# Optimization experiments

Measured on AMD Instinct MI355X. Metric: run time of the kernel, lower is better.

Reference implementation:

```python
import jax, jax.numpy as jnp
import numpy as np

N = 100000   # nodes
E = 600000   # edges per edge set
D = 128      # d_graph_layer (= num_features)
ED = 3       # edge_dim
DF = 512     # d_FC_layer
B = 64       # graphs in batch
C = 2        # num_classes
NL = 3       # n_graph_layer (stacked convs)


def _lin_params(key, out_d, in_d, bias=True, scale=0.05):
    kw, kb = jax.random.split(key)
    w = jax.random.normal(kw, (out_d, in_d), dtype=jnp.float32) * scale
    b = jax.random.normal(kb, (out_d,), dtype=jnp.float32) * scale if bias else None
    return w, b


def setup_inputs() -> dict:
    key = jax.random.key(0)
    ks = jax.random.split(key, 32)
    inp = {}
    inp["x"] = jax.random.normal(ks[0], (N, D), dtype=jnp.float32)
    inp["edge_index1"] = jax.random.randint(ks[1], (2, E), 0, N, dtype=jnp.int64) if jax.config.jax_enable_x64 else jax.random.randint(ks[1], (2, E), 0, N).astype(jnp.int32)
    inp["edge_index2"] = jax.random.randint(ks[2], (2, E), 0, N).astype(inp["edge_index1"].dtype)
    inp["edge_attr1"] = jax.random.normal(ks[3], (E, ED), dtype=jnp.float32)
    inp["edge_attr2"] = jax.random.normal(ks[4], (E, ED), dtype=jnp.float32)
    inp["flexible_idx"] = jnp.ones((N,), dtype=bool)
    inp["batchs"] = jnp.sort(jax.random.randint(ks[5], (N,), 0, B)).astype(inp["edge_index1"].dtype)

    # conv1 params: lin_query, lin_key, lin_value (with bias), lin_edge (no bias), lin_skip (bias)
    inp["c1_wq"], inp["c1_bq"] = _lin_params(ks[6], D, D)
    inp["c1_wk"], inp["c1_bk"] = _lin_params(ks[7], D, D)
    inp["c1_wv"], inp["c1_bv"] = _lin_params(ks[8], D, D)
    inp["c1_we"], _ = _lin_params(ks[9], D, ED, bias=False)
    inp["c1_ws"], inp["c1_bs"] = _lin_params(ks[10], D, D)

    # stacked convs: [NL, ...]
    def stack(kbase, out_d, in_d, bias=True):
        ws, bs = [], []
        for i in range(NL):
            w, b = _lin_params(jax.random.fold_in(kbase, i), out_d, in_d, bias)
            ws.append(w)
            bs.append(b)
        return jnp.stack(ws), (jnp.stack(bs) if bias else None)
    inp["cs_wq"], inp["cs_bq"] = stack(ks[11], D, D)
    inp["cs_wk"], inp["cs_bk"] = stack(ks[12], D, D)
    inp["cs_wv"], inp["cs_bv"] = stack(ks[13], D, D)
    inp["cs_we"], _ = stack(ks[14], D, ED, bias=False)
    inp["cs_ws"], inp["cs_bs"] = stack(ks[15], D, D)

    inp["lin0_w"], inp["lin0_b"] = _lin_params(ks[16], DF, D)
    inp["lin1_w"], inp["lin1_b"] = _lin_params(ks[17], DF, DF)
    inp["lin3_w"], inp["lin3_b"] = _lin_params(ks[18], C, DF)
    return inp


def _tconv(x, edge_index, edge_attr, wq, bq, wk, bk, wv, bv, we, ws, bs):
    """PyG TransformerConv, heads=1, concat=True, root_weight=True, edge_dim=3."""
    n = x.shape[0]
    src, dst = edge_index[0], edge_index[1]
    q = x @ wq.T + bq                     # [N, D]
    k = x @ wk.T + bk                     # [N, D]
    v = x @ wv.T + bv                     # [N, D]
    e = edge_attr @ we.T                  # [E, D]
    k_e = k[src] + e                      # [E, D]
    v_e = v[src] + e                      # [E, D]
    scale = 1.0 / jnp.sqrt(jnp.asarray(x.shape[-1], x.dtype))
    logits = jnp.sum(q[dst] * k_e, axis=-1) * scale   # [E]
    m = jax.ops.segment_max(logits, dst, num_segments=n)
    w = jnp.exp(logits - m[dst])
    den = jax.ops.segment_sum(w, dst, num_segments=n)
    alpha = w / (den[dst] + 1e-16)        # softmax over incoming edges
    out = jax.ops.segment_sum(alpha[:, None] * v_e, dst, num_segments=n)
    return out + x @ ws.T + bs            # root / skip connection


def reference(x, edge_index1, edge_index2, edge_attr1, edge_attr2, flexible_idx, batchs,
              c1_wq, c1_bq, c1_wk, c1_bk, c1_wv, c1_bv, c1_we, c1_ws, c1_bs,
              cs_wq, cs_bq, cs_wk, cs_bk, cs_wv, cs_bv, cs_we, cs_ws, cs_bs,
              lin0_w, lin0_b, lin1_w, lin1_b, lin3_w, lin3_b):
    # conv1 applied to both edge structures; x = relu(conv(g2)) - relu(conv(g1))
    x1 = jax.nn.relu(_tconv(x, edge_index1, edge_attr1, c1_wq, c1_bq, c1_wk, c1_bk, c1_wv, c1_bv, c1_we, c1_ws, c1_bs))
    x2 = jax.nn.relu(_tconv(x, edge_index2, edge_attr2, c1_wq, c1_bq, c1_wk, c1_bk, c1_wv, c1_bv, c1_we, c1_ws, c1_bs))
    h = x2 - x1                           # dropout_rate=0 -> identity
    for i in range(NL):
        x1 = jax.nn.relu(_tconv(h, edge_index1, edge_attr1, cs_wq[i], cs_bq[i], cs_wk[i], cs_bk[i], cs_wv[i], cs_bv[i], cs_we[i], cs_ws[i], cs_bs[i]))
        x2 = jax.nn.relu(_tconv(h, edge_index2, edge_attr2, cs_wq[i], cs_bq[i], cs_wk[i], cs_bk[i], cs_wv[i], cs_bv[i], cs_we[i], cs_ws[i], cs_bs[i]))
        h = x2 - x1
    # global_mean_pool (flexible=False)
    sums = jax.ops.segment_sum(h, batchs, num_segments=B)               # [B, D]
    cnt = jax.ops.segment_sum(jnp.ones((h.shape[0],), h.dtype), batchs, num_segments=B)
    g = sums / jnp.maximum(cnt, 1.0)[:, None]
    g = jax.nn.relu(g @ lin0_w.T + lin0_b)
    g = jax.nn.relu(g @ lin1_w.T + lin1_b)
    logits = g @ lin3_w.T + lin3_b
    return jax.nn.log_softmax(logits, axis=1)   # last == 'log'
```

## Files before the change

### kernel.cpp

```cpp
#include <hip/hip_runtime.h>

#define NNODES 100000
#define NEDGES 600000
#define DIM    128
#define NB     64
#define DFC    512
#define NB1    391

typedef __attribute__((ext_vector_type(8))) short short8v;
typedef __attribute__((ext_vector_type(4))) float float4v;

__device__ __forceinline__ float bf2f(unsigned short u) {
    return __uint_as_float((unsigned)u << 16);
}
__device__ __forceinline__ unsigned short f2bf(float f) {
    unsigned u = __float_as_uint(f);
    return (unsigned short)((u + 0x7FFF + ((u >> 16) & 1)) >> 16);
}

__global__ __launch_bounds__(256) void wsplit_kernel(
    const float* __restrict__ c1q, const float* __restrict__ c1k,
    const float* __restrict__ c1v, const float* __restrict__ c1s,
    const float* __restrict__ csq, const float* __restrict__ csk,
    const float* __restrict__ csv, const float* __restrict__ css,
    short* __restrict__ whi, short* __restrict__ wlo)
{
    int t = blockIdx.x * 256 + threadIdx.x;
    int mat = t >> 11;
    int tt = t & 2047;
    int lane = tt & 63, nt = (tt >> 6) & 7, ks = tt >> 9;
    int li = mat >> 2, mm = mat & 3;
    const float* W;
    if (li == 0) W = (mm == 0) ? c1q : (mm == 1) ? c1k : (mm == 2) ? c1v : c1s;
    else {
        const float* base = (mm == 0) ? csq : (mm == 1) ? csk : (mm == 2) ? csv : css;
        W = base + (size_t)(li - 1) * 16384;
    }
    int n = nt * 16 + (lane & 15);
    int k0 = ks * 32 + (lane >> 4) * 8;
    size_t ob = (size_t)mat * 16384 + (size_t)((ks * 8 + nt) * 64 + lane) * 8;
#pragma unroll
    for (int j = 0; j < 8; ++j) {
        float w = W[n * 128 + k0 + j];
        unsigned ub = __float_as_uint(w);
        float lo = w - __uint_as_float(ub & 0xFFFF0000u);
        whi[ob + j] = (short)(ub >> 16);
        wlo[ob + j] = (short)(__float_as_uint(lo) >> 16);
    }
}

__global__ __launch_bounds__(256) void qkvs_mfma_kernel(
    const float* __restrict__ x,
    const short* __restrict__ whi, const short* __restrict__ wlo,
    const float* __restrict__ bq, const float* __restrict__ bk,
    const float* __restrict__ bv, const float* __restrict__ bs,
    float* __restrict__ q, unsigned short* __restrict__ k16,
    unsigned short* __restrict__ v16,
    float* __restrict__ o1, float* __restrict__ h2)
{
    const int lane = threadIdx.x & 63;
    const int m = threadIdx.x >> 6;
    const int r0 = blockIdx.x * 32;
    const int lrow = lane & 15;
    const int lgrp = lane >> 4;

    float4v acc[2][8] = {};
    const short* Whi = whi + (size_t)m * 16384;
    const short* Wlo = wlo + (size_t)m * 16384;

    for (int ks = 0; ks < 4; ++ks) {
        short8v ahi[2], alo[2];
#pragma unroll
        for (int mt = 0; mt < 2; ++mt) {
            const float* xp = x + (size_t)(r0 + mt * 16 + lrow) * DIM + ks * 32 + lgrp * 8;
            float4 xa = *(const float4*)xp;
            float4 xb = *(const float4*)(xp + 4);
            float xs[8] = {xa.x, xa.y, xa.z, xa.w, xb.x, xb.y, xb.z, xb.w};
#pragma unroll
            for (int j = 0; j < 8; ++j) {
                unsigned ub = __float_as_uint(xs[j]);
                float lo = xs[j] - __uint_as_float(ub & 0xFFFF0000u);
                ahi[mt][j] = (short)(ub >> 16);
                alo[mt][j] = (short)(__float_as_uint(lo) >> 16);
            }
        }
        const short* bh = Whi + (size_t)((ks * 8) * 64 + lane) * 8;
        const short* bl = Wlo + (size_t)((ks * 8) * 64 + lane) * 8;
#pragma unroll
        for (int nt = 0; nt < 8; ++nt) {
            short8v bhi = *(const short8v*)(bh + (size_t)nt * 512);
            short8v blo = *(const short8v*)(bl + (size_t)nt * 512);
#pragma unroll
            for (int mt = 0; mt < 2; ++mt) {
                acc[mt][nt] = __builtin_amdgcn_mfma_f32_16x16x32_bf16(ahi[mt], bhi, acc[mt][nt], 0, 0, 0);
                acc[mt][nt] = __builtin_amdgcn_mfma_f32_16x16x32_bf16(ahi[mt], blo, acc[mt][nt], 0, 0, 0);
                acc[mt][nt] = __builtin_amdgcn_mfma_f32_16x16x32_bf16(alo[mt], bhi, acc[mt][nt], 0, 0, 0);
            }
        }
    }

    __syncthreads();

    const float* bias = (m == 0) ? bq : (m == 1) ? bk : (m == 2) ? bv : bs;
#pragma unroll
    for (int nt = 0; nt < 8; ++nt) {
        float bvv = bias[nt * 16 + lrow];
#pragma unroll
        for (int mt = 0; mt < 2; ++mt) {
#pragma unroll
            for (int i = 0; i < 4; ++i) {
                int row = r0 + mt * 16 + lgrp * 4 + i;
                float val = acc[mt][nt][i] + bvv;
                size_t off = (size_t)row * DIM + nt * 16 + lrow;
                if (m == 0) q[off] = val;
                else if (m == 1) k16[off] = f2bf(val);
                else if (m == 2) v16[off] = f2bf(val);
                else { o1[off] = val; h2[off] = val; }
            }
        }
    }
}

__global__ __launch_bounds__(256) void hist_kernel(const int* __restrict__ ei,
                                                   int* __restrict__ deg) {
    int e = blockIdx.x * 256 + threadIdx.x;
    if (e < NEDGES) atomicAdd(&deg[ei[NEDGES + e]], 1);
}

__global__ __launch_bounds__(256) void scan1_kernel(const int* __restrict__ deg,
                                                    int* __restrict__ excl,
                                                    int* __restrict__ bsum) {
    __shared__ int s[256];
    const int tid = threadIdx.x;
    const int i = blockIdx.x * 256 + tid;
    const int v = (i < NNODES) ? deg[i] : 0;
    s[tid] = v;
    __syncthreads();
    for (int off = 1; off < 256; off <<= 1) {
        int t = (tid >= off) ? s[tid - off] : 0;
        __syncthreads();
        s[tid] += t;
        __syncthreads();
    }
    if (i < NNODES) excl[i] = s[tid] - v;
    if (tid == 255) bsum[blockIdx.x] = s[255];
}

__global__ __launch_bounds__(512) void scan2_kernel(int* __restrict__ bsum) {
    __shared__ int s[512];
    const int tid = threadIdx.x;
    const int v = (tid < NB1) ? bsum[tid] : 0;
    s[tid] = v;
    __syncthreads();
    for (int off = 1; off < 512; off <<= 1) {
        int t = (tid >= off) ? s[tid - off] : 0;
        __syncthreads();
        s[tid] += t;
        __syncthreads();
    }
    if (tid < NB1) bsum[tid] = s[tid] - v;
}

__global__ __launch_bounds__(256) void scan3_kernel(const int* __restrict__ excl,
                                                    const int* __restrict__ bsum,
                                                    int* __restrict__ rowptr) {
    const int i = blockIdx.x * 256 + threadIdx.x;
    if (i < NNODES) rowptr[i] = excl[i] + bsum[blockIdx.x];
    if (i == 0) rowptr[NNODES] = NEDGES;
}

__global__ __launch_bounds__(256) void scatter_edges_kernel(
    const int* __restrict__ ei, const int* __restrict__ rowptr,
    int* __restrict__ fill, int2* __restrict__ sse) {
    int e = blockIdx.x * 256 + threadIdx.x;
    if (e >= NEDGES) return;
    int dst = ei[NEDGES + e];
    int pos = rowptr[dst] + atomicAdd(&fill[dst], 1);
    sse[pos] = make_int2(ei[e], e);
}

__global__ __launch_bounds__(256) void attn_aggregate_kernel(
    const int* __restrict__ rowptr1, const int2* __restrict__ sse1,
    const float* __restrict__ ea1,
    const int* __restrict__ rowptr2, const int2* __restrict__ sse2,
    const float* __restrict__ ea2,
    const float* __restrict__ we,
    const float* __restrict__ q, const unsigned short* __restrict__ k16,
    const unsigned short* __restrict__ v16,
    float* __restrict__ o1, float* __restrict__ o2)
{
    const int wave = threadIdx.x >> 6;
    const int lane = threadIdx.x & 63;
    const int idx = blockIdx.x * 4 + wave;
    if (idx >= 2 * NNODES) return;
    const int g = (idx >= NNODES) ? 1 : 0;
    const int d = idx - (g ? NNODES : 0);

    const int*   rowptr = g ? rowptr2 : rowptr1;
    const int2*  sse    = g ? sse2 : sse1;
    const float* ea     = g ? ea2 : ea1;
    float*       out    = g ? o2 : o1;

    const int p0 = rowptr[d], p1 = rowptr[d + 1];
    if (p0 == p1) return;

    const int c0 = lane, c1 = lane + 64;
    const float w00 = we[c0 * 3 + 0], w01 = we[c0 * 3 + 1], w02 = we[c0 * 3 + 2];
    const float w10 = we[c1 * 3 + 0], w11 = we[c1 * 3 + 1], w12 = we[c1 * 3 + 2];
    const float scale = 0.08838834764831845f;
    const float q0 = q[(size_t)d * DIM + c0] * scale;
    const float q1 = q[(size_t)d * DIM + c1] * scale;

    float m = -INFINITY, den = 0.f, a0 = 0.f, a1 = 0.f;

    for (int p = p0; p < p1; p += 4) {
        const int nn = p1 - p;
        float l[4], vv0[4], vv1[4];
#pragma unroll
        for (int j = 0; j < 4; ++j) {
            if (j < nn) {
                const int2 sv = sse[p + j];
                const int src = sv.x;
                const float ea0 = ea[sv.y * 3 + 0];
                const float ea1v = ea[sv.y * 3 + 1];
                const float ea2v = ea[sv.y * 3 + 2];
                const float ep0 = fmaf(ea0, w00, fmaf(ea1v, w01, ea2v * w02));
                const float ep1 = fmaf(ea0, w10, fmaf(ea1v, w11, ea2v * w12));
                const unsigned short* kp = k16 + (size_t)src * DIM;
                const unsigned short* vp = v16 + (size_t)src * DIM;
                const float k0 = bf2f(kp[c0]) + ep0;
                const float k1 = bf2f(kp[c1]) + ep1;
                vv0[j] = bf2f(vp[c0]) + ep0;
                vv1[j] = bf2f(vp[c1]) + ep1;
                l[j] = fmaf(q0, k0, q1 * k1);
            } else {
                l[j] = -INFINITY;
                vv0[j] = 0.f;
                vv1[j] = 0.f;
            }
        }
#pragma unroll
        for (int off = 32; off > 0; off >>= 1) {
#pragma unroll
            for (int j = 0; j < 4; ++j) l[j] += __shfl_xor(l[j], off, 64);
        }
        const float cm = fmaxf(fmaxf(l[0], l[1]), fmaxf(l[2], l[3]));
        const float mn = fmaxf(m, cm);
        const float sc = __expf(m - mn);
        const float e0 = __expf(l[0] - mn), e1 = __expf(l[1] - mn);
        const float e2 = __expf(l[2] - mn), e3 = __expf(l[3] - mn);
        den = den * sc + ((e0 + e1) + (e2 + e3));
        a0 = a0 * sc + ((e0 * vv0[0] + e1 * vv0[1]) + (e2 * vv0[2] + e3 * vv0[3]));
        a1 = a1 * sc + ((e0 * vv1[0] + e1 * vv1[1]) + (e2 * vv1[2] + e3 * vv1[3]));
        m = mn;
    }
    const float inv = 1.f / (den + 1e-16f);
    out[(size_t)d * DIM + c0] += a0 * inv;
    out[(size_t)d * DIM + c1] += a1 * inv;
}

__global__ __launch_bounds__(256) void combine_kernel(
    const float4* __restrict__ o1, float4* __restrict__ h)
{
    const int i = blockIdx.x * 256 + threadIdx.x;
    float4 a = o1[i];
    float4 b = h[i];
    float4 r;
    r.x = fmaxf(b.x, 0.f) - fmaxf(a.x, 0.f);
    r.y = fmaxf(b.y, 0.f) - fmaxf(a.y, 0.f);
    r.z = fmaxf(b.z, 0.f) - fmaxf(a.z, 0.f);
    r.w = fmaxf(b.w, 0.f) - fmaxf(a.w, 0.f);
    h[i] = r;
}

__global__ __launch_bounds__(256) void pool_kernel(
    const float* __restrict__ h, const int* __restrict__ batchs,
    float* __restrict__ sums, float* __restrict__ cnt)
{
    const int sub = threadIdx.x >> 7;
    const int c = threadIdx.x & 127;
    int n0 = blockIdx.x * 32 + sub * 16;
    int nend = n0 + 16;
    if (nend > NNODES) nend = NNODES;
    float acc = 0.f, ccnt = 0.f;
    int curb = -1;
    for (int nd = n0; nd < nend; ++nd) {
        int b = batchs[nd];
        if (b != curb) {
            if (curb >= 0) {
                atomicAdd(&sums[curb * DIM + c], acc);
                if (c == 0) atomicAdd(&cnt[curb], ccnt);
            }
            acc = 0.f; ccnt = 0.f; curb = b;
        }
        acc += h[(size_t)nd * DIM + c];
        ccnt += 1.f;
    }
    if (curb >= 0) {
        atomicAdd(&sums[curb * DIM + c], acc);
        if (c == 0) atomicAdd(&cnt[curb], ccnt);
    }
}

__global__ __launch_bounds__(256) void head_kernel(
    const float* __restrict__ sums, const float* __restrict__ cnt,
    const float* __restrict__ l0w, const float* __restrict__ l0b,
    const float* __restrict__ l1w, const float* __restrict__ l1b,
    const float* __restrict__ l3w, const float* __restrict__ l3b,
    float* __restrict__ out)
{
    __shared__ float g[DIM];
    __shared__ float h0[DFC];
    __shared__ float h1[DFC];
    __shared__ float lg[2];
    const int b = blockIdx.x;
    const int tid = threadIdx.x;
    const float c = fmaxf(cnt[b], 1.0f);
    if (tid < DIM) g[tid] = sums[b * DIM + tid] / c;
    __syncthreads();
    for (int o = tid; o < DFC; o += 256) {
        float acc = l0b[o];
        for (int kk = 0; kk < DIM; ++kk) acc = fmaf(g[kk], l0w[o * DIM + kk], acc);
        h0[o] = fmaxf(acc, 0.f);
    }
    __syncthreads();
    for (int o = tid; o < DFC; o += 256) {
        float acc = l1b[o];
        for (int kk = 0; kk < DFC; ++kk) acc = fmaf(h0[kk], l1w[o * DFC + kk], acc);
        h1[o] = fmaxf(acc, 0.f);
    }
    __syncthreads();
    if (tid < 2) {
        float acc = l3b[tid];
        for (int kk = 0; kk < DFC; ++kk) acc = fmaf(h1[kk], l3w[tid * DFC + kk], acc);
        lg[tid] = acc;
    }
    __syncthreads();
    if (tid == 0) {
        float l0 = lg[0], l1v = lg[1];
        float mx = fmaxf(l0, l1v);
        float lse = mx + logf(expf(l0 - mx) + expf(l1v - mx));
        out[b * 2 + 0] = l0 - lse;
        out[b * 2 + 1] = l1v - lse;
    }
}

extern "C" void kernel_launch(void* const* d_in, const int* in_sizes, int n_in,
                              void* d_out, int out_size, void* d_ws, size_t ws_size,
                              hipStream_t stream)
{
    const float* x      = (const float*)d_in[0];
    const int*   ei1    = (const int*)d_in[1];
    const int*   ei2    = (const int*)d_in[2];
    const float* ea1    = (const float*)d_in[3];
    const float* ea2    = (const float*)d_in[4];
    const int*   batchs = (const int*)d_in[6];

    float* ws_f = (float*)d_ws;
    const size_t ND = (size_t)NNODES * DIM;
    float* q    = ws_f;
    float* o1   = q + ND;
    float* h    = o1 + ND;
    unsigned short* k16 = (unsigned short*)(h + ND);
    unsigned short* v16 = k16 + ND;
    float* sums = (float*)(v16 + ND);
    float* cnt  = sums + NB * DIM;
    short* whi  = (short*)(cnt + NB);
    short* wlo  = whi + 16 * 16384;
    int*   ip   = (int*)(wlo + 16 * 16384);
    int*  rowptr1 = ip;
    int*  rowptr2 = rowptr1 + (NNODES + 1);
    int*  pad     = rowptr2 + (NNODES + 1);
    int2* sse1    = (int2*)(pad + ((((size_t)(pad)) & 4) ? 1 : 1));
    {
        size_t off = (size_t)(pad - ip);
        if (off & 1) pad += 1;
        sse1 = (int2*)pad;
    }
    int2* sse2    = sse1 + NEDGES;
    int*  deg     = (int*)(sse2 + NEDGES);
    int*  excl    = deg + NNODES;
    int*  bsum    = excl + NNODES;

    wsplit_kernel<<<128, 256, 0, stream>>>(
        (const float*)d_in[7], (const float*)d_in[9],
        (const float*)d_in[11], (const float*)d_in[14],
        (const float*)d_in[16], (const float*)d_in[18],
        (const float*)d_in[20], (const float*)d_in[23],
        whi, wlo);

    for (int gi = 0; gi < 2; ++gi) {
        const int* ei = gi ? ei2 : ei1;
        int*  rowptr = gi ? rowptr2 : rowptr1;
        int2* sse    = gi ? sse2 : sse1;
        hipMemsetAsync(deg, 0, NNODES * sizeof(int), stream);
        hist_kernel<<<(NEDGES + 255) / 256, 256, 0, stream>>>(ei, deg);
        scan1_kernel<<<NB1, 256, 0, stream>>>(deg, excl, bsum);
        scan2_kernel<<<1, 512, 0, stream>>>(bsum);
        scan3_kernel<<<NB1, 256, 0, stream>>>(excl, bsum, rowptr);
        hipMemsetAsync(excl, 0, NNODES * sizeof(int), stream);
        scatter_edges_kernel<<<(NEDGES + 255) / 256, 256, 0, stream>>>(ei, rowptr, excl, sse);
    }

    const float* xin = x;
    for (int li = 0; li < 4; ++li) {
        const float *bq_, *bk_, *bv_, *bs_, *we_;
        if (li == 0) {
            bq_ = (const float*)d_in[8];
            bk_ = (const float*)d_in[10];
            bv_ = (const float*)d_in[12];
            bs_ = (const float*)d_in[15];
            we_ = (const float*)d_in[13];
        } else {
            int i = li - 1;
            bq_ = (const float*)d_in[17] + (size_t)i * DIM;
            bk_ = (const float*)d_in[19] + (size_t)i * DIM;
            bv_ = (const float*)d_in[21] + (size_t)i * DIM;
            bs_ = (const float*)d_in[24] + (size_t)i * DIM;
            we_ = (const float*)d_in[22] + (size_t)i * DIM * 3;
        }

        qkvs_mfma_kernel<<<NNODES / 32, 256, 0, stream>>>(
            xin, whi + (size_t)li * 4 * 16384, wlo + (size_t)li * 4 * 16384,
            bq_, bk_, bv_, bs_, q, k16, v16, o1, h);

        attn_aggregate_kernel<<<(2 * NNODES + 3) / 4, 256, 0, stream>>>(
            rowptr1, sse1, ea1, rowptr2, sse2, ea2,
            we_, q, k16, v16, o1, h);

        combine_kernel<<<(int)(ND / 1024), 256, 0, stream>>>((const float4*)o1, (float4*)h);
        xin = h;
    }

    hipMemsetAsync(sums, 0, NB * DIM * sizeof(float), stream);
    hipMemsetAsync(cnt, 0, NB * sizeof(float), stream);
    pool_kernel<<<(NNODES + 31) / 32, 256, 0, stream>>>(h, batchs, sums, cnt);
    head_kernel<<<NB, 256, 0, stream>>>(sums, cnt,
        (const float*)d_in[25], (const float*)d_in[26],
        (const float*)d_in[27], (const float*)d_in[28],
        (const float*)d_in[29], (const float*)d_in[30],
        (float*)d_out);
}
```

Baseline: 1.814 ms.

## Fuse both edge-set aggregations and relu-difference combine into one attention kernel

Each wave now handles one destination node for both edge sets, reusing its q, skip and edge-weight loads, and writes h = relu(s+agg2) - relu(s+agg1) directly. This drops the separate combine kernel and the double write of the skip output. Edge attributes are permuted into CSR order during preprocessing, so the attention loop reads them contiguously instead of gathering through the edge id. The cost is half as many waves in flight and serialised per-node work across the two edge sets, which may reduce latency hiding.

```diff
diff --git a/kernel.cpp b/kernel.cpp
--- a/kernel.cpp
+++ b/kernel.cpp
@@ -55,8 +55,7 @@
     const float* __restrict__ bq, const float* __restrict__ bk,
     const float* __restrict__ bv, const float* __restrict__ bs,
     float* __restrict__ q, unsigned short* __restrict__ k16,
-    unsigned short* __restrict__ v16,
-    float* __restrict__ o1, float* __restrict__ h2)
+    unsigned short* __restrict__ v16, float* __restrict__ s)
 {
     const int lane = threadIdx.x & 63;
     const int m = threadIdx.x >> 6;
@@ -98,8 +97,6 @@
             }
         }
     }
-
-    __syncthreads();
 
     const float* bias = (m == 0) ? bq : (m == 1) ? bk : (m == 2) ? bv : bs;
 #pragma unroll
@@ -115,7 +112,7 @@
                 if (m == 0) q[off] = val;
                 else if (m == 1) k16[off] = f2bf(val);
                 else if (m == 2) v16[off] = f2bf(val);
-                else { o1[off] = val; h2[off] = val; }
+                else s[off] = val;
             }
         }
     }
@@ -170,60 +167,39 @@
 }
 
 __global__ __launch_bounds__(256) void scatter_edges_kernel(
-    const int* __restrict__ ei, const int* __restrict__ rowptr,
-    int* __restrict__ fill, int2* __restrict__ sse) {
+    const int* __restrict__ ei, const float* __restrict__ ea,
+    const int* __restrict__ rowptr, int* __restrict__ fill,
+    int* __restrict__ ssrc, float* __restrict__ eas) {
     int e = blockIdx.x * 256 + threadIdx.x;
     if (e >= NEDGES) return;
     int dst = ei[NEDGES + e];
     int pos = rowptr[dst] + atomicAdd(&fill[dst], 1);
-    sse[pos] = make_int2(ei[e], e);
-}
-
-__global__ __launch_bounds__(256) void attn_aggregate_kernel(
-    const int* __restrict__ rowptr1, const int2* __restrict__ sse1,
-    const float* __restrict__ ea1,
-    const int* __restrict__ rowptr2, const int2* __restrict__ sse2,
-    const float* __restrict__ ea2,
-    const float* __restrict__ we,
-    const float* __restrict__ q, const unsigned short* __restrict__ k16,
-    const unsigned short* __restrict__ v16,
-    float* __restrict__ o1, float* __restrict__ o2)
-{
-    const int wave = threadIdx.x >> 6;
-    const int lane = threadIdx.x & 63;
-    const int idx = blockIdx.x * 4 + wave;
-    if (idx >= 2 * NNODES) return;
-    const int g = (idx >= NNODES) ? 1 : 0;
-    const int d = idx - (g ? NNODES : 0);
-
-    const int*   rowptr = g ? rowptr2 : rowptr1;
-    const int2*  sse    = g ? sse2 : sse1;
-    const float* ea     = g ? ea2 : ea1;
-    float*       out    = g ? o2 : o1;
-
+    ssrc[pos] = ei[e];
+    eas[pos * 3 + 0] = ea[e * 3 + 0];
+    eas[pos * 3 + 1] = ea[e * 3 + 1];
+    eas[pos * 3 + 2] = ea[e * 3 + 2];
+}
+
+__device__ __forceinline__ void edge_pass(
+    const int* __restrict__ rowptr, const int* __restrict__ ssrc,
+    const float* __restrict__ eas,
+    const unsigned short* __restrict__ k16, const unsigned short* __restrict__ v16,
+    int d, int c0, int c1,
+    float w00, float w01, float w02, float w10, float w11, float w12,
+    float q0, float q1, float& r0, float& r1)
+{
     const int p0 = rowptr[d], p1 = rowptr[d + 1];
-    if (p0 == p1) return;
-
-    const int c0 = lane, c1 = lane + 64;
-    const float w00 = we[c0 * 3 + 0], w01 = we[c0 * 3 + 1], w02 = we[c0 * 3 + 2];
-    const float w10 = we[c1 * 3 + 0], w11 = we[c1 * 3 + 1], w12 = we[c1 * 3 + 2];
-    const float scale = 0.08838834764831845f;
-    const float q0 = q[(size_t)d * DIM + c0] * scale;
-    const float q1 = q[(size_t)d * DIM + c1] * scale;
-
     float m = -INFINITY, den = 0.f, a0 = 0.f, a1 = 0.f;
-
     for (int p = p0; p < p1; p += 4) {
         const int nn = p1 - p;
         float l[4], vv0[4], vv1[4];
 #pragma unroll
         for (int j = 0; j < 4; ++j) {
             if (j < nn) {
-                const int2 sv = sse[p + j];
-                const int src = sv.x;
-                const float ea0 = ea[sv.y * 3 + 0];
-                const float ea1v = ea[sv.y * 3 + 1];
-                const float ea2v = ea[sv.y * 3 + 2];
+                const int src = ssrc[p + j];
+                const float ea0 = eas[(p + j) * 3 + 0];
+                const float ea1v = eas[(p + j) * 3 + 1];
+                const float ea2v = eas[(p + j) * 3 + 2];
                 const float ep0 = fmaf(ea0, w00, fmaf(ea1v, w01, ea2v * w02));
                 const float ep1 = fmaf(ea0, w10, fmaf(ea1v, w11, ea2v * w12));
                 const unsigned short* kp = k16 + (size_t)src * DIM;
@@ -255,22 +231,40 @@
         m = mn;
     }
     const float inv = 1.f / (den + 1e-16f);
-    out[(size_t)d * DIM + c0] += a0 * inv;
-    out[(size_t)d * DIM + c1] += a1 * inv;
-}
-
-__global__ __launch_bounds__(256) void combine_kernel(
-    const float4* __restrict__ o1, float4* __restrict__ h)
-{
-    const int i = blockIdx.x * 256 + threadIdx.x;
-    float4 a = o1[i];
-    float4 b = h[i];
-    float4 r;
-    r.x = fmaxf(b.x, 0.f) - fmaxf(a.x, 0.f);
-    r.y = fmaxf(b.y, 0.f) - fmaxf(a.y, 0.f);
-    r.z = fmaxf(b.z, 0.f) - fmaxf(a.z, 0.f);
-    r.w = fmaxf(b.w, 0.f) - fmaxf(a.w, 0.f);
-    h[i] = r;
+    r0 = a0 * inv;
+    r1 = a1 * inv;
+}
+
+__global__ __launch_bounds__(256) void attn_aggregate_kernel(
+    const int* __restrict__ rowptr1, const int* __restrict__ ssrc1,
+    const float* __restrict__ eas1,
+    const int* __restrict__ rowptr2, const int* __restrict__ ssrc2,
+    const float* __restrict__ eas2,
+    const float* __restrict__ we,
+    const float* __restrict__ q, const unsigned short* __restrict__ k16,
+    const unsigned short* __restrict__ v16,
+    const float* __restrict__ s, float* __restrict__ h)
+{
+    const int wave = threadIdx.x >> 6;
+    const int lane = threadIdx.x & 63;
+    const int d = blockIdx.x * 4 + wave;
+    const int c0 = lane, c1 = lane + 64;
+    const float w00 = we[c0 * 3 + 0], w01 = we[c0 * 3 + 1], w02 = we[c0 * 3 + 2];
+    const float w10 = we[c1 * 3 + 0], w11 = we[c1 * 3 + 1], w12 = we[c1 * 3 + 2];
+    const float scale = 0.08838834764831845f;
+    const float q0 = q[(size_t)d * DIM + c0] * scale;
+    const float q1 = q[(size_t)d * DIM + c1] * scale;
+    const float s0 = s[(size_t)d * DIM + c0];
+    const float s1 = s[(size_t)d * DIM + c1];
+
+    float r1_0, r1_1, r2_0, r2_1;
+    edge_pass(rowptr1, ssrc1, eas1, k16, v16, d, c0, c1,
+              w00, w01, w02, w10, w11, w12, q0, q1, r1_0, r1_1);
+    edge_pass(rowptr2, ssrc2, eas2, k16, v16, d, c0, c1,
+              w00, w01, w02, w10, w11, w12, q0, q1, r2_0, r2_1);
+
+    h[(size_t)d * DIM + c0] = fmaxf(s0 + r2_0, 0.f) - fmaxf(s0 + r1_0, 0.f);
+    h[(size_t)d * DIM + c1] = fmaxf(s1 + r2_1, 0.f) - fmaxf(s1 + r1_1, 0.f);
 }
 
 __global__ __launch_bounds__(256) void pool_kernel(
@@ -359,28 +353,24 @@
     float* ws_f = (float*)d_ws;
     const size_t ND = (size_t)NNODES * DIM;
     float* q    = ws_f;
-    float* o1   = q + ND;
-    float* h    = o1 + ND;
+    float* sbuf = q + ND;
+    float* h    = sbuf + ND;
     unsigned short* k16 = (unsigned short*)(h + ND);
     unsigned short* v16 = k16 + ND;
     float* sums = (float*)(v16 + ND);
     float* cnt  = sums + NB * DIM;
     short* whi  = (short*)(cnt + NB);
     short* wlo  = whi + 16 * 16384;
-    int*   ip   = (int*)(wlo + 16 * 16384);
-    int*  rowptr1 = ip;
-    int*  rowptr2 = rowptr1 + (NNODES + 1);
-    int*  pad     = rowptr2 + (NNODES + 1);
-    int2* sse1    = (int2*)(pad + ((((size_t)(pad)) & 4) ? 1 : 1));
-    {
-        size_t off = (size_t)(pad - ip);
-        if (off & 1) pad += 1;
-        sse1 = (int2*)pad;
-    }
-    int2* sse2    = sse1 + NEDGES;
-    int*  deg     = (int*)(sse2 + NEDGES);
-    int*  excl    = deg + NNODES;
-    int*  bsum    = excl + NNODES;
+    float* eas1 = (float*)(wlo + 16 * 16384);
+    float* eas2 = eas1 + (size_t)NEDGES * 3;
+    int*   ip   = (int*)(eas2 + (size_t)NEDGES * 3);
+    int* rowptr1 = ip;
+    int* rowptr2 = rowptr1 + (NNODES + 1);
+    int* ssrc1   = rowptr2 + (NNODES + 1);
+    int* ssrc2   = ssrc1 + NEDGES;
+    int* deg     = ssrc2 + NEDGES;
+    int* excl    = deg + NNODES;
+    int* bsum    = excl + NNODES;
 
     wsplit_kernel<<<128, 256, 0, stream>>>(
         (const float*)d_in[7], (const float*)d_in[9],
@@ -390,16 +380,18 @@
         whi, wlo);
 
     for (int gi = 0; gi < 2; ++gi) {
-        const int* ei = gi ? ei2 : ei1;
-        int*  rowptr = gi ? rowptr2 : rowptr1;
-        int2* sse    = gi ? sse2 : sse1;
+        const int*   ei = gi ? ei2 : ei1;
+        const float* ea = gi ? ea2 : ea1;
+        int*   rowptr = gi ? rowptr2 : rowptr1;
+        int*   ssrc   = gi ? ssrc2 : ssrc1;
+        float* eas    = gi ? eas2 : eas1;
         hipMemsetAsync(deg, 0, NNODES * sizeof(int), stream);
         hist_kernel<<<(NEDGES + 255) / 256, 256, 0, stream>>>(ei, deg);
         scan1_kernel<<<NB1, 256, 0, stream>>>(deg, excl, bsum);
         scan2_kernel<<<1, 512, 0, stream>>>(bsum);
         scan3_kernel<<<NB1, 256, 0, stream>>>(excl, bsum, rowptr);
         hipMemsetAsync(excl, 0, NNODES * sizeof(int), stream);
-        scatter_edges_kernel<<<(NEDGES + 255) / 256, 256, 0, stream>>>(ei, rowptr, excl, sse);
+        scatter_edges_kernel<<<(NEDGES + 255) / 256, 256, 0, stream>>>(ei, ea, rowptr, excl, ssrc, eas);
     }
 
     const float* xin = x;
@@ -422,13 +414,12 @@
 
         qkvs_mfma_kernel<<<NNODES / 32, 256, 0, stream>>>(
             xin, whi + (size_t)li * 4 * 16384, wlo + (size_t)li * 4 * 16384,
-            bq_, bk_, bv_, bs_, q, k16, v16, o1, h);
-
-        attn_aggregate_kernel<<<(2 * NNODES + 3) / 4, 256, 0, stream>>>(
-            rowptr1, sse1, ea1, rowptr2, sse2, ea2,
-            we_, q, k16, v16, o1, h);
-
-        combine_kernel<<<(int)(ND / 1024), 256, 0, stream>>>((const float4*)o1, (float4*)h);
+            bq_, bk_, bv_, bs_, q, k16, v16, sbuf);
+
+        attn_aggregate_kernel<<<NNODES / 4, 256, 0, stream>>>(
+            rowptr1, ssrc1, eas1, rowptr2, ssrc2, eas2,
+            we_, q, k16, v16, sbuf, h);
+
         xin = h;
     }
 
```

Measured after the change: 1.590 ms. -12.4%, faster.
